# Performance work log

Hardware: AMD Instinct MI355X
Metric: run time of the kernel (lower is better)

## Reference

```python
import jax, jax.numpy as jnp
import numpy as np


def _lstm_cell(x, h, c, Wih, Whh, bih, bhh):
    # PyTorch LSTMCell gate order: i, f, g, o
    g = x @ Wih.T + h @ Whh.T + bih + bhh
    i, f, gg, o = jnp.split(g, 4, axis=-1)
    c = jax.nn.sigmoid(f) * c + jax.nn.sigmoid(i) * jnp.tanh(gg)
    h = jax.nn.sigmoid(o) * jnp.tanh(c)
    return h, c


def setup_inputs() -> dict:
    F, H, B, Te, Td = 64, 128, 1024, 168, 24
    shapes = {
        'input_p_q': (B, Te, F), 'label_p': (B, Td),
        'Wi_w': (H, F), 'Wi_b': (H,), 'We_w': (H, 2 * H),
        'Vd_w': (F, H), 'Vd_b': (F,),
        'enc_Wih': (4 * H, F), 'enc_Whh': (4 * H, H), 'enc_bih': (4 * H,), 'enc_bhh': (4 * H,),
        'mid_Wih': (4 * H, H), 'mid_Whh': (4 * H, H), 'mid_bih': (4 * H,), 'mid_bhh': (4 * H,),
        'Wx_w': (H, H), 'Wx_b': (H,), 'Wh_w': (H, 2 * H),
        'V_w': (1, H), 'V_b': (1,),
        'dec_Wih': (4 * H, H), 'dec_Whh': (4 * H, H), 'dec_bih': (4 * H,), 'dec_bhh': (4 * H,),
        'reg_w': (1, H), 'reg_b': (1,),
    }
    key = jax.random.key(0)
    ks = jax.random.split(key, len(shapes))
    out = {}
    for k, (name, shp) in zip(ks, shapes.items()):
        scale = 1.0 if name in ('input_p_q', 'label_p') else 0.05
        out[name] = jax.random.normal(k, shp, jnp.float32) * scale
    return out


def reference(input_p_q, label_p, Wi_w, Wi_b, We_w, Vd_w, Vd_b,
              enc_Wih, enc_Whh, enc_bih, enc_bhh,
              mid_Wih, mid_Whh, mid_bih, mid_bhh,
              Wx_w, Wx_b, Wh_w, V_w, V_b,
              dec_Wih, dec_Whh, dec_bih, dec_bhh, reg_w, reg_b):
    B, Te, F = input_p_q.shape
    H = Wi_w.shape[0]
    Td = label_p.shape[1]
    h0 = jnp.zeros((B, H), input_p_q.dtype)

    # ---- spatial-attention LSTMCell encoder ----
    xs = jnp.transpose(input_p_q, (1, 0, 2))  # [Te, B, F]

    def enc_step(carry, x_t):
        h, c = carry
        s = jnp.tanh(jnp.concatenate([h, c], axis=1) @ We_w.T
                     + x_t @ Wi_w.T + Wi_b) @ Vd_w.T + Vd_b  # [B, F]
        x_in = x_t * jax.nn.softmax(s, axis=1)
        h, c = _lstm_cell(x_in, h, c, enc_Wih, enc_Whh, enc_bih, enc_bhh)
        return (h, c), h

    _, mid = jax.lax.scan(enc_step, (h0, h0), xs)  # [Te, B, H]

    # ---- single-layer nn.LSTM (LSTM_mid), zero init state ----
    def mid_step(carry, x_t):
        h, c = carry
        h, c = _lstm_cell(x_t, h, c, mid_Wih, mid_Whh, mid_bih, mid_bhh)
        return (h, c), h

    (hi, ci), mid_out = jax.lax.scan(mid_step, (h0, h0), mid)
    mid_out = jnp.transpose(mid_out, (1, 0, 2))  # [B, Te, H]

    # ---- temporal-attention LSTMCell decoder (no softmax on scores, faithful) ----
    wx_mid = mid_out @ Wx_w.T + Wx_b  # [B, Te, H]

    def dec_step(carry, _):
        hi, ci = carry
        q = jnp.concatenate([hi, ci], axis=1) @ Wh_w.T  # [B, H]
        s = jnp.tanh(q[:, None, :] + wx_mid) @ V_w.T + V_b  # [B, Te, 1]
        dec_in = jnp.einsum('bt,bth->bh', s[..., 0], mid_out)
        hi, ci = _lstm_cell(dec_in, hi, ci, dec_Wih, dec_Whh, dec_bih, dec_bhh)
        return (hi, ci), hi

    _, dec = jax.lax.scan(dec_step, (hi, ci), None, length=Td)  # [Td, B, H]
    out = jnp.transpose(dec, (1, 0, 2)) @ reg_w.T + reg_b  # [B, Td, 1]
    return out[..., 0]
```

## Files before the change

kernel.cpp:

```cpp
#include <hip/hip_runtime.h>

#define B_   1024
#define TE   168
#define TD   24
#define F_   64
#define H_   128
#define H2_  256
#define G_   512

#define OFF_WhT    0
#define OFF_dWihT  16384
#define OFF_dWhhT  49152
#define OFF_ENCB   81920
#define OFF_MIDB   82432
#define OFF_DECB   82944
#define OFF_W16    83456
#define W16_We     0
#define W16_Wi     32768
#define W16_Vd     40960
#define W16_eWih   49152
#define W16_eWhh   81920
#define W16_mWih   147456
#define W16_mWhh   212992
#define W16_Wx     278528
#define W16_TOT    294912
#define OFF_MID    230912
#define OFF_WX     (OFF_MID + (B_*TE*H_)/2)
#define OFF_STH    (OFF_WX  + (B_*TE*H_)/2)
#define OFF_STC    (OFF_STH + B_*H_)
#define WS_FLOATS  (OFF_STC + B_*H_)

typedef _Float16 h2 __attribute__((ext_vector_type(2)));
typedef _Float16 h8 __attribute__((ext_vector_type(8)));
typedef _Float16 f16x8 __attribute__((ext_vector_type(8)));
typedef float    f32x4 __attribute__((ext_vector_type(4)));

__device__ __forceinline__ float fexp2(float x) { return __builtin_amdgcn_exp2f(x); }
__device__ __forceinline__ float frcp(float x)  { return __builtin_amdgcn_rcpf(x); }
#define LOG2E 1.4426950408889634f

__device__ __forceinline__ float sigm(float x) {
    return frcp(1.f + fexp2(-LOG2E * x));
}
__device__ __forceinline__ float tanh_fast(float x) {
    float e = fexp2(2.f * LOG2E * x);
    return 1.f - 2.f * frcp(e + 1.f);
}

__device__ __forceinline__ float fdot2(h2 a, h2 b, float c) {
#if __has_builtin(__builtin_amdgcn_fdot2)
    return __builtin_amdgcn_fdot2(a, b, c, false);
#else
    return c + (float)a[0] * (float)b[0] + (float)a[1] * (float)b[1];
#endif
}
__device__ __forceinline__ void fma4(float4& g, const float4 wv, const float s) {
    g.x = __builtin_fmaf(wv.x, s, g.x);
    g.y = __builtin_fmaf(wv.y, s, g.y);
    g.z = __builtin_fmaf(wv.z, s, g.z);
    g.w = __builtin_fmaf(wv.w, s, g.w);
}

#define SH(V,I)  __builtin_shufflevector(V, V, 2*(I), 2*(I)+1)
#define SL(CG)   (4*((CG) + ((CG)>>3)))

#define DPAIR2(LOV, HIV, R0, R1) { \
    h2 c0=SH(LOV,0), c1=SH(LOV,1), c2=SH(LOV,2), c3=SH(LOV,3); \
    h2 c4=SH(HIV,0), c5=SH(HIV,1), c6=SH(HIV,2), c7=SH(HIV,3); \
    a00.x=fdot2(R0,c0,a00.x); a00.y=fdot2(R0,c1,a00.y); a00.z=fdot2(R0,c2,a00.z); a00.w=fdot2(R0,c3,a00.w); \
    a01.x=fdot2(R0,c4,a01.x); a01.y=fdot2(R0,c5,a01.y); a01.z=fdot2(R0,c6,a01.z); a01.w=fdot2(R0,c7,a01.w); \
    a10.x=fdot2(R1,c0,a10.x); a10.y=fdot2(R1,c1,a10.y); a10.z=fdot2(R1,c2,a10.z); a10.w=fdot2(R1,c3,a10.w); \
    a11.x=fdot2(R1,c4,a11.x); a11.y=fdot2(R1,c5,a11.y); a11.z=fdot2(R1,c6,a11.z); a11.w=fdot2(R1,c7,a11.w); \
}

__device__ __forceinline__ f32x4 mfma16(f16x8 a, f16x8 b, f32x4 c) {
    return __builtin_amdgcn_mfma_f32_16x16x32_f16(a, b, c, 0, 0, 0);
}

struct PrepArgs {
    const float *We, *Wi, *Vd, *eWih, *eWhh, *eBih, *eBhh,
                *mWih, *mWhh, *mBih, *mBhh, *Wx, *Wh, *dWih, *dWhh, *dBih, *dBhh;
};

__global__ void prep_kernel(PrepArgs a, float* __restrict__ ws) {
    int sec  = blockIdx.x >> 2;
    int base = (blockIdx.x & 3) * blockDim.x + threadIdx.x;
    const int stride = blockDim.x * 4;
    _Float16* w16 = (_Float16*)(ws + OFF_W16);

    if (sec <= 2) {
        const float* src = (sec == 0) ? a.Wh : (sec == 1) ? a.dWih : a.dWhh;
        int R = (sec == 0) ? 128 : 512;
        int C = (sec == 0) ? 256 : 128;
        int off = (sec == 0) ? OFF_WhT : (sec == 1) ? OFF_dWihT : OFF_dWhhT;
        int n = R * C;
        _Float16* hd = (_Float16*)(ws + off);
        for (int o = base; o < n; o += stride) {
            int r = o % R, c = o / R;
            hd[(c >> 1) * 2 * R + 2 * r + (c & 1)] = (_Float16)src[r * C + c];
        }
    } else if (sec == 3) {
        for (int i = base; i < 512; i += stride) ws[OFF_ENCB + i] = a.eBih[i] + a.eBhh[i];
    } else if (sec == 4) {
        for (int i = base; i < 512; i += stride) ws[OFF_MIDB + i] = a.mBih[i] + a.mBhh[i];
    } else if (sec == 5) {
        for (int i = base; i < 512; i += stride) ws[OFF_DECB + i] = a.dBih[i] + a.dBhh[i];
    } else if (sec <= 13) {
        const int dsto[8] = {W16_We, W16_Wi, W16_Vd, W16_eWih, W16_eWhh, W16_mWih, W16_mWhh, W16_Wx};
        const int cnt[8]  = {32768, 8192, 8192, 32768, 65536, 65536, 65536, 16384};
        const float* srcs[8] = {a.We, a.Wi, a.Vd, a.eWih, a.eWhh, a.mWih, a.mWhh, a.Wx};
        int k = sec - 6;
        const float* s = srcs[k];
        _Float16* d = w16 + dsto[k];
        int n = cnt[k];
        for (int i = base; i < n; i += stride) d[i] = (_Float16)s[i];
    }
}

__global__ __launch_bounds__(512, 1) void enc_kernel(
    const float* __restrict__ x_all,
    const float* __restrict__ Wi_b,
    const float* __restrict__ Vd_b,
    float* __restrict__ ws)
{
    __shared__ __align__(16) _Float16 m1In[16][328];
    __shared__ __align__(16) _Float16 encIn[16][200];
    __shared__ __align__(16) _Float16 avT[16][136];
    __shared__ __align__(16) float sS[16][68];
    __shared__ __align__(16) float xf[16][64];
    __shared__ __align__(16) float cE[16][132];
    __shared__ float bWi[H_], bVd[F_], bE[G_];

    const int tid  = threadIdx.x;
    const int wave = tid >> 6;
    const int lane = tid & 63;
    const int g    = lane >> 4;
    const int cc   = lane & 15;
    const int b0   = blockIdx.x * 16;
    const int col  = wave * 16 + cc;

    for (int i = tid; i < 16 * 328; i += 512) ((_Float16*)m1In)[i]  = (_Float16)0.f;
    for (int i = tid; i < 16 * 200; i += 512) ((_Float16*)encIn)[i] = (_Float16)0.f;
    for (int i = tid; i < 16 * 132; i += 512) ((float*)cE)[i] = 0.f;
    if (tid < H_) bWi[tid] = Wi_b[tid];
    if (tid < F_) bVd[tid] = Vd_b[tid];
    bE[tid] = ws[OFF_ENCB + tid];
    if (tid < 256) {
        int m = tid >> 4, c4 = (tid & 15) * 4;
        float4 v = *(const float4*)&x_all[((size_t)(b0 + m) * TE + 0) * F_ + c4];
        *(float4*)&xf[m][c4] = v;
        m1In[m][256 + c4]     = (_Float16)v.x;
        m1In[m][256 + c4 + 1] = (_Float16)v.y;
        m1In[m][256 + c4 + 2] = (_Float16)v.z;
        m1In[m][256 + c4 + 3] = (_Float16)v.w;
    }

    const _Float16* w16 = (const _Float16*)(ws + OFF_W16);
    f16x8 wWe[8], wWi[2], wVd[4], wIh[4][2], wHh[4][4];
    {
        const _Float16* p = w16 + W16_We + (size_t)col * 256 + 8 * g;
        #pragma unroll
        for (int ks = 0; ks < 8; ++ks) wWe[ks] = *(const f16x8*)(p + ks * 32);
        const _Float16* p2 = w16 + W16_Wi + (size_t)col * 64 + 8 * g;
        wWi[0] = *(const f16x8*)(p2);
        wWi[1] = *(const f16x8*)(p2 + 32);
        if (wave < 4) {
            const _Float16* p3 = w16 + W16_Vd + (size_t)col * 128 + 8 * g;
            #pragma unroll
            for (int ks = 0; ks < 4; ++ks) wVd[ks] = *(const f16x8*)(p3 + ks * 32);
        } else {
            #pragma unroll
            for (int ks = 0; ks < 4; ++ks) wVd[ks] = f16x8{};
        }
        #pragma unroll
        for (int q = 0; q < 4; ++q) {
            const _Float16* pi = w16 + W16_eWih + (size_t)(q * 128 + col) * 64 + 8 * g;
            wIh[q][0] = *(const f16x8*)(pi);
            wIh[q][1] = *(const f16x8*)(pi + 32);
            const _Float16* ph = w16 + W16_eWhh + (size_t)(q * 128 + col) * 128 + 8 * g;
            #pragma unroll
            for (int ks = 0; ks < 4; ++ks) wHh[q][ks] = *(const f16x8*)(ph + ks * 32);
        }
    }
    _Float16* hencG = (_Float16*)(ws + OFF_MID);
    __syncthreads();

    float4 xr = make_float4(0.f, 0.f, 0.f, 0.f);

    for (int t = 0; t < TE; ++t) {
        {
            f16x8 aF[10];
            #pragma unroll
            for (int ks = 0; ks < 10; ++ks)
                aF[ks] = *(const f16x8*)&m1In[cc][ks * 32 + 8 * g];
            f32x4 acc = {0.f, 0.f, 0.f, 0.f};
            #pragma unroll
            for (int ks = 0; ks < 8; ++ks)
                acc = mfma16(aF[ks], wWe[ks], acc);
            acc = mfma16(aF[8], wWi[0], acc);
            acc = mfma16(aF[9], wWi[1], acc);
            float bw = bWi[col];
            #pragma unroll
            for (int r = 0; r < 4; ++r)
                avT[4 * g + r][col] = (_Float16)tanh_fast(acc[r] + bw);
        }
        __syncthreads();

        if (wave < 4) {
            f16x8 aF[4];
            #pragma unroll
            for (int ks = 0; ks < 4; ++ks)
                aF[ks] = *(const f16x8*)&avT[cc][ks * 32 + 8 * g];
            f32x4 acc = {0.f, 0.f, 0.f, 0.f};
            #pragma unroll
            for (int ks = 0; ks < 4; ++ks)
                acc = mfma16(aF[ks], wVd[ks], acc);
            float bv = bVd[col];
            #pragma unroll
            for (int r = 0; r < 4; ++r)
                sS[4 * g + r][col] = acc[r] + bv;
        } else if (t + 1 < TE) {
            int q = tid - 256, m = q >> 4, c4 = (q & 15) * 4;
            xr = *(const float4*)&x_all[((size_t)(b0 + m) * TE + (t + 1)) * F_ + c4];
        }
        __syncthreads();

        {
            int m = tid >> 5, c = tid & 31;
            float v0 = sS[m][c], v1 = sS[m][c + 32];
            float mx = fmaxf(v0, v1);
            #pragma unroll
            for (int off = 16; off > 0; off >>= 1) mx = fmaxf(mx, __shfl_xor(mx, off, 64));
            float e0 = fexp2((v0 - mx) * LOG2E);
            float e1 = fexp2((v1 - mx) * LOG2E);
            float sm = e0 + e1;
            #pragma unroll
            for (int off = 16; off > 0; off >>= 1) sm += __shfl_xor(sm, off, 64);
            float rs = frcp(sm);
            encIn[m][c]      = (_Float16)(xf[m][c]      * e0 * rs);
            encIn[m][c + 32] = (_Float16)(xf[m][c + 32] * e1 * rs);
        }
        __syncthreads();

        f32x4 ge[4];
        {
            f16x8 aF[6];
            #pragma unroll
            for (int ks = 0; ks < 6; ++ks)
                aF[ks] = *(const f16x8*)&encIn[cc][ks * 32 + 8 * g];
            #pragma unroll
            for (int q = 0; q < 4; ++q) {
                f32x4 acc = {0.f, 0.f, 0.f, 0.f};
                acc = mfma16(aF[0], wIh[q][0], acc);
                acc = mfma16(aF[1], wIh[q][1], acc);
                #pragma unroll
                for (int ks = 0; ks < 4; ++ks)
                    acc = mfma16(aF[2 + ks], wHh[q][ks], acc);
                ge[q] = acc;
            }
        }
        __syncthreads();
        {
            float bi = bE[col], bf = bE[col + 128], bg = bE[col + 256], bo = bE[col + 384];
            #pragma unroll
            for (int r = 0; r < 4; ++r) {
                int m = 4 * g + r;
                float gi = ge[0][r] + bi, gf = ge[1][r] + bf,
                      gg = ge[2][r] + bg, go = ge[3][r] + bo;
                float cn = sigm(gf) * cE[m][col] + sigm(gi) * tanh_fast(gg);
                float h  = sigm(go) * tanh_fast(cn);
                cE[m][col] = cn;
                _Float16 hh = (_Float16)h;
                encIn[m][64 + col] = hh;
                m1In[m][col]       = hh;
                m1In[m][128 + col] = (_Float16)cn;
                hencG[((size_t)(b0 + m) * TE + t) * H_ + col] = hh;
            }
            if (tid >= 256 && t + 1 < TE) {
                int q = tid - 256, m = q >> 4, c4 = (q & 15) * 4;
                *(float4*)&xf[m][c4] = xr;
                m1In[m][256 + c4]     = (_Float16)xr.x;
                m1In[m][256 + c4 + 1] = (_Float16)xr.y;
                m1In[m][256 + c4 + 2] = (_Float16)xr.z;
                m1In[m][256 + c4 + 3] = (_Float16)xr.w;
            }
        }
        __syncthreads();
    }
}

__global__ __launch_bounds__(512, 1) void mid_kernel(
    const float* __restrict__ Wx_b,
    float* __restrict__ ws)
{
    __shared__ __align__(16) _Float16 midIn[16][264];
    __shared__ __align__(16) float cM[16][132];
    __shared__ float bM[G_], bWx[H_];

    const int tid  = threadIdx.x;
    const int wave = tid >> 6;
    const int lane = tid & 63;
    const int g    = lane >> 4;
    const int cc   = lane & 15;
    const int b0   = blockIdx.x * 16;
    const int col  = wave * 16 + cc;

    for (int i = tid; i < 16 * 264; i += 512) ((_Float16*)midIn)[i] = (_Float16)0.f;
    for (int i = tid; i < 16 * 132; i += 512) ((float*)cM)[i] = 0.f;
    if (tid < H_) bWx[tid] = Wx_b[tid];
    bM[tid] = ws[OFF_MIDB + tid];

    const _Float16* w16 = (const _Float16*)(ws + OFF_W16);
    f16x8 wIhB[4][4], wHhB[4][4], wWx[4];
    {
        #pragma unroll
        for (int q = 0; q < 4; ++q) {
            const _Float16* pi = w16 + W16_mWih + (size_t)(q * 128 + col) * 128 + 8 * g;
            const _Float16* ph = w16 + W16_mWhh + (size_t)(q * 128 + col) * 128 + 8 * g;
            #pragma unroll
            for (int ks = 0; ks < 4; ++ks) {
                wIhB[q][ks] = *(const f16x8*)(pi + ks * 32);
                wHhB[q][ks] = *(const f16x8*)(ph + ks * 32);
            }
        }
        const _Float16* px = w16 + W16_Wx + (size_t)col * 128 + 8 * g;
        #pragma unroll
        for (int ks = 0; ks < 4; ++ks) wWx[ks] = *(const f16x8*)(px + ks * 32);
    }

    _Float16* hencG = (_Float16*)(ws + OFF_MID);
    _Float16* wxH   = (_Float16*)(ws + OFF_WX);
    __syncthreads();

    if (tid < 256) {
        int m = tid >> 4, s8 = (tid & 15) * 8;
        *(f16x8*)&midIn[m][s8] = *(const f16x8*)&hencG[((size_t)(b0 + m) * TE + 0) * H_ + s8];
    }
    __syncthreads();

    f16x8 hpre = {};
    f32x4 accx = {0.f, 0.f, 0.f, 0.f};

    for (int t = 0; t < TE; ++t) {
        f32x4 gm[4];
        {
            f16x8 aF[8];
            #pragma unroll
            for (int ks = 0; ks < 8; ++ks)
                aF[ks] = *(const f16x8*)&midIn[cc][ks * 32 + 8 * g];
            #pragma unroll
            for (int q = 0; q < 4; ++q) {
                f32x4 acc = {0.f, 0.f, 0.f, 0.f};
                #pragma unroll
                for (int ks = 0; ks < 4; ++ks)
                    acc = mfma16(aF[ks], wIhB[q][ks], acc);
                #pragma unroll
                for (int ks = 0; ks < 4; ++ks)
                    acc = mfma16(aF[4 + ks], wHhB[q][ks], acc);
                gm[q] = acc;
            }
            if (t > 0) {
                f32x4 acc = {0.f, 0.f, 0.f, 0.f};
                #pragma unroll
                for (int ks = 0; ks < 4; ++ks)
                    acc = mfma16(aF[4 + ks], wWx[ks], acc);
                accx = acc;
            }
        }
        if (tid < 256 && t + 1 < TE) {
            int m = tid >> 4, s8 = (tid & 15) * 8;
            hpre = *(const f16x8*)&hencG[((size_t)(b0 + m) * TE + (t + 1)) * H_ + s8];
        }
        __syncthreads();

        {
            float bi = bM[col], bf = bM[col + 128], bg = bM[col + 256], bo = bM[col + 384];
            float bw = bWx[col];
            #pragma unroll
            for (int r = 0; r < 4; ++r) {
                int m = 4 * g + r;
                float gi = gm[0][r] + bi, gf = gm[1][r] + bf,
                      gg = gm[2][r] + bg, go = gm[3][r] + bo;
                float cn = sigm(gf) * cM[m][col] + sigm(gi) * tanh_fast(gg);
                float h  = sigm(go) * tanh_fast(cn);
                cM[m][col] = cn;
                _Float16 hh = (_Float16)h;
                midIn[m][128 + col] = hh;
                hencG[((size_t)(b0 + m) * TE + t) * H_ + col] = hh;
                if (t > 0)
                    wxH[((size_t)(b0 + m) * TE + (t - 1)) * H_ + col] = (_Float16)(accx[r] + bw);
            }
            if (tid < 256 && t + 1 < TE) {
                int m = tid >> 4, s8 = (tid & 15) * 8;
                *(f16x8*)&midIn[m][s8] = hpre;
            }
        }
        __syncthreads();
    }

    {
        f16x8 ax[4];
        #pragma unroll
        for (int ks = 0; ks < 4; ++ks)
            ax[ks] = *(const f16x8*)&midIn[cc][128 + ks * 32 + 8 * g];
        f32x4 acc = {0.f, 0.f, 0.f, 0.f};
        #pragma unroll
        for (int ks = 0; ks < 4; ++ks)
            acc = mfma16(ax[ks], wWx[ks], acc);
        float bw = bWx[col];
        #pragma unroll
        for (int r = 0; r < 4; ++r) {
            int m = 4 * g + r;
            wxH[((size_t)(b0 + m) * TE + (TE - 1)) * H_ + col] = (_Float16)(acc[r] + bw);
        }
    }
    for (int idx = tid; idx < 2048; idx += 512) {
        int m = idx >> 7, j = idx & 127;
        ws[OFF_STH + (b0 + m) * H_ + j] = (float)midIn[m][128 + j];
        ws[OFF_STC + (b0 + m) * H_ + j] = cM[m][j];
    }
}

#define QP_ 132

__global__ __launch_bounds__(512, 2) void dec_kernel(
    const float* __restrict__ Vw_in,
    const float* __restrict__ Vb_in,
    const float* __restrict__ rw_in,
    const float* __restrict__ rb_in,
    const float* __restrict__ ws,
    float* __restrict__ out)
{
    __shared__ __align__(16) float scr[9216];
    __shared__ __align__(16) float hc2[2][H2_];
    __shared__ __align__(16) float qv[2][QP_];
    __shared__ __align__(16) float sb[2][TE];
    __shared__ __align__(16) float dinp[8][2][H_];
    __shared__ float bD[G_], Vw[H_], rw[H_];

    const int tid = threadIdx.x;
    const int b0  = blockIdx.x * 2;
    const float Vb = Vb_in[0], rb = rb_in[0];

    {
        int r = tid >> 8, c = tid & 255;
        hc2[r][c] = (c < H_) ? ws[OFF_STH + (b0 + r) * H_ + c]
                             : ws[OFF_STC + (b0 + r) * H_ + (c - H_)];
    }
    if (tid < H_) { Vw[tid] = Vw_in[tid]; rw[tid] = rw_in[tid]; }
    bD[tid] = ws[OFF_DECB + tid];
    __syncthreads();

    const h8* WhH2  = (const h8*)(ws + OFF_WhT);
    const h8* dWih2 = (const h8*)(ws + OFF_dWihT);
    const h8* dWhh2 = (const h8*)(ws + OFF_dWhhT);
    const h8* wx8   = (const h8*)(ws + OFF_WX);
    typedef _Float16 h4 __attribute__((ext_vector_type(4)));
    const h4* mid4 = (const h4*)(ws + OFF_MID);

    for (int td = 0; td < TD; ++td) {
        {
            int cg = tid & 15, ks = tid >> 4;
            int p0 = ks * 4;
            float4 a00 = make_float4(0.f,0.f,0.f,0.f), a01 = a00, a10 = a00, a11 = a00;
            #pragma unroll
            for (int i = 0; i < 4; ++i) {
                int p = p0 + i;
                h8 lo = WhH2[p * 32 + cg * 2];
                h8 hi = WhH2[p * 32 + cg * 2 + 1];
                h2 r0; r0[0] = (_Float16)hc2[0][2*p]; r0[1] = (_Float16)hc2[0][2*p+1];
                h2 r1; r1[0] = (_Float16)hc2[1][2*p]; r1[1] = (_Float16)hc2[1][2*p+1];
                DPAIR2(lo, hi, r0, r1);
            }
            int sl = SL(cg);
            float* sp = scr + ks * 288;
            *(float4*)(sp +       sl) = a00; *(float4*)(sp +  72 + sl) = a01;
            *(float4*)(sp + 144 + sl) = a10; *(float4*)(sp + 216 + sl) = a11;
        }
        __syncthreads();
        if (tid < 256) {
            int j = tid & 127, r = tid >> 7;
            int e = j & 7, cgj = j >> 3;
            int idx = r * 144 + ((e < 4) ? SL(cgj) + e : 72 + SL(cgj) + (e - 4));
            float v = 0.f;
            #pragma unroll
            for (int ks = 0; ks < 32; ++ks) v += scr[ks * 288 + idx];
            qv[r][j] = v;
        }
        __syncthreads();

        for (int task = tid; task < 2 * TE; task += 512) {
            int r = (task >= TE) ? 1 : 0;
            int tp = task - r * TE;
            const h8* wxr = wx8 + ((size_t)(b0 + r) * TE + tp) * 16;
            float acc = Vb;
            #pragma unroll 4
            for (int kk = 0; kk < 16; ++kk) {
                h8 hv = wxr[kk];
                int j = kk * 8;
                float4 q0 = *(const float4*)&qv[r][j], q1 = *(const float4*)&qv[r][j + 4];
                float4 v0 = *(const float4*)&Vw[j],    v1 = *(const float4*)&Vw[j + 4];
                acc += tanh_fast(q0.x + (float)hv[0]) * v0.x + tanh_fast(q0.y + (float)hv[1]) * v0.y
                     + tanh_fast(q0.z + (float)hv[2]) * v0.z + tanh_fast(q0.w + (float)hv[3]) * v0.w;
                acc += tanh_fast(q1.x + (float)hv[4]) * v1.x + tanh_fast(q1.y + (float)hv[5]) * v1.y
                     + tanh_fast(q1.z + (float)hv[6]) * v1.z + tanh_fast(q1.w + (float)hv[7]) * v1.w;
            }
            sb[r][tp] = acc;
        }
        __syncthreads();

        {
            int ts = tid >> 6, r = (tid >> 5) & 1, cg = tid & 31;
            int t0 = ts * 21;
            float4 a = make_float4(0.f, 0.f, 0.f, 0.f);
            #pragma unroll 3
            for (int tp = t0; tp < t0 + 21; ++tp) {
                float s = sb[r][tp];
                h4 m = mid4[((size_t)(b0 + r) * TE + tp) * 32 + cg];
                float4 mf;
                mf.x = (float)m[0]; mf.y = (float)m[1]; mf.z = (float)m[2]; mf.w = (float)m[3];
                fma4(a, mf, s);
            }
            *(float4*)&dinp[ts][r][cg * 4] = a;
        }
        __syncthreads();
        if (tid < 256) {
            int j = tid & 127, r = tid >> 7;
            qv[r][j] = ((dinp[0][r][j] + dinp[1][r][j]) + (dinp[2][r][j] + dinp[3][r][j]))
                     + ((dinp[4][r][j] + dinp[5][r][j]) + (dinp[6][r][j] + dinp[7][r][j]));
        }
        __syncthreads();

        {
            int cg = tid & 63, ks = tid >> 6;
            int p0 = ks * 8;
            float4 a00 = make_float4(0.f,0.f,0.f,0.f), a01 = a00, a10 = a00, a11 = a00;
            #pragma unroll 4
            for (int i = 0; i < 8; ++i) {
                int p = p0 + i;
                h8 lo = dWih2[p * 128 + cg * 2];
                h8 hi = dWih2[p * 128 + cg * 2 + 1];
                h2 r0; r0[0] = (_Float16)qv[0][2*p]; r0[1] = (_Float16)qv[0][2*p+1];
                h2 r1; r1[0] = (_Float16)qv[1][2*p]; r1[1] = (_Float16)qv[1][2*p+1];
                DPAIR2(lo, hi, r0, r1);
            }
            #pragma unroll 4
            for (int i = 0; i < 8; ++i) {
                int p = p0 + i;
                h8 lo = dWhh2[p * 128 + cg * 2];
                h8 hi = dWhh2[p * 128 + cg * 2 + 1];
                h2 r0; r0[0] = (_Float16)hc2[0][2*p]; r0[1] = (_Float16)hc2[0][2*p+1];
                h2 r1; r1[0] = (_Float16)hc2[1][2*p]; r1[1] = (_Float16)hc2[1][2*p+1];
                DPAIR2(lo, hi, r0, r1);
            }
            int sl = SL(cg);
            float* sp = scr + ks * 1152;
            *(float4*)(sp +       sl) = a00; *(float4*)(sp + 288 + sl) = a01;
            *(float4*)(sp + 576 + sl) = a10; *(float4*)(sp + 864 + sl) = a11;
        }
        __syncthreads();

        if (tid < 256) {
            int j = tid & 127, r = tid >> 7;
            int e = j & 7, cgj = j >> 3;
            int i0, i1, i2, i3;
            {
                int c0 = cgj, c1 = 16 + cgj, c2 = 32 + cgj, c3 = 48 + cgj;
                i0 = (e < 4) ? SL(c0) + e : 288 + SL(c0) + (e - 4);
                i1 = (e < 4) ? SL(c1) + e : 288 + SL(c1) + (e - 4);
                i2 = (e < 4) ? SL(c2) + e : 288 + SL(c2) + (e - 4);
                i3 = (e < 4) ? SL(c3) + e : 288 + SL(c3) + (e - 4);
            }
            const float* sp = scr + r * 576;
            float gi = bD[j], gf = bD[j + 128], gg = bD[j + 256], go = bD[j + 384];
            #pragma unroll
            for (int ks = 0; ks < 8; ++ks) {
                const float* p = sp + ks * 1152;
                gi += p[i0]; gf += p[i1]; gg += p[i2]; go += p[i3];
            }
            float c = sigm(gf) * hc2[r][H_ + j] + sigm(gi) * tanh_fast(gg);
            float h = sigm(go) * tanh_fast(c);
            hc2[r][H_ + j] = c; hc2[r][j] = h;
        }
        __syncthreads();

        if (tid < 128) {
            int r = tid >> 6, lane = tid & 63;
            float v = hc2[r][lane] * rw[lane] + hc2[r][lane + 64] * rw[lane + 64];
            for (int off = 32; off > 0; off >>= 1) v += __shfl_xor(v, off, 64);
            if (lane == 0) out[(b0 + r) * TD + td] = v + rb;
        }
    }
}

extern "C" void kernel_launch(void* const* d_in, const int* in_sizes, int n_in,
                              void* d_out, int out_size, void* d_ws, size_t ws_size,
                              hipStream_t stream)
{
    (void)in_sizes; (void)n_in; (void)out_size;
    if (ws_size < (size_t)WS_FLOATS * sizeof(float)) return;

    const float* x_all = (const float*)d_in[0];
    const float* Wi_b  = (const float*)d_in[3];
    const float* Vd_b  = (const float*)d_in[6];
    const float* Wx_b  = (const float*)d_in[16];
    const float* V_w   = (const float*)d_in[18];
    const float* V_b   = (const float*)d_in[19];
    const float* reg_w = (const float*)d_in[24];
    const float* reg_b = (const float*)d_in[25];
    float* ws  = (float*)d_ws;
    float* out = (float*)d_out;

    PrepArgs pa{
        (const float*)d_in[4],
        (const float*)d_in[2],
        (const float*)d_in[5],
        (const float*)d_in[7],
        (const float*)d_in[8],
        (const float*)d_in[9],
        (const float*)d_in[10],
        (const float*)d_in[11],
        (const float*)d_in[12],
        (const float*)d_in[13],
        (const float*)d_in[14],
        (const float*)d_in[15],
        (const float*)d_in[17],
        (const float*)d_in[20],
        (const float*)d_in[21],
        (const float*)d_in[22],
        (const float*)d_in[23]
    };

    prep_kernel<<<56, 256, 0, stream>>>(pa, ws);
    enc_kernel<<<64, 512, 0, stream>>>(x_all, Wi_b, Vd_b, ws);
    mid_kernel<<<64, 512, 0, stream>>>(Wx_b, ws);
    dec_kernel<<<512, 512, 0, stream>>>(V_w, V_b, reg_w, reg_b, ws, out);
}
```

Baseline: 1.288 ms.

## Fuse encoder and mid LSTM into one producer-consumer kernel with flag sync

New measurement: 1.079 ms. 16.3% less time.

```diff
diff --git a/kernel.cpp b/kernel.cpp
--- a/kernel.cpp
+++ b/kernel.cpp
@@ -82,7 +82,7 @@
                 *mWih, *mWhh, *mBih, *mBhh, *Wx, *Wh, *dWih, *dWhh, *dBih, *dBhh;
 };
 
-__global__ void prep_kernel(PrepArgs a, float* __restrict__ ws) {
+__global__ void prep_kernel(PrepArgs a, float* __restrict__ ws, int* __restrict__ flags) {
     int sec  = blockIdx.x >> 2;
     int base = (blockIdx.x & 3) * blockDim.x + threadIdx.x;
     const int stride = blockDim.x * 4;
@@ -105,6 +105,7 @@
         for (int i = base; i < 512; i += stride) ws[OFF_MIDB + i] = a.mBih[i] + a.mBhh[i];
     } else if (sec == 5) {
         for (int i = base; i < 512; i += stride) ws[OFF_DECB + i] = a.dBih[i] + a.dBhh[i];
+        for (int i = base; i < 64; i += stride) flags[i] = 0;
     } else if (sec <= 13) {
         const int dsto[8] = {W16_We, W16_Wi, W16_Vd, W16_eWih, W16_eWhh, W16_mWih, W16_mWhh, W16_Wx};
         const int cnt[8]  = {32768, 8192, 8192, 32768, 65536, 65536, 65536, 16384};
@@ -117,307 +118,318 @@
     }
 }
 
-__global__ __launch_bounds__(512, 1) void enc_kernel(
+__global__ __launch_bounds__(512, 1) void enc_mid_kernel(
     const float* __restrict__ x_all,
     const float* __restrict__ Wi_b,
     const float* __restrict__ Vd_b,
-    float* __restrict__ ws)
+    const float* __restrict__ Wx_b,
+    float* __restrict__ ws,
+    int* __restrict__ flags)
 {
-    __shared__ __align__(16) _Float16 m1In[16][328];
-    __shared__ __align__(16) _Float16 encIn[16][200];
-    __shared__ __align__(16) _Float16 avT[16][136];
-    __shared__ __align__(16) float sS[16][68];
-    __shared__ __align__(16) float xf[16][64];
-    __shared__ __align__(16) float cE[16][132];
-    __shared__ float bWi[H_], bVd[F_], bE[G_];
-
     const int tid  = threadIdx.x;
     const int wave = tid >> 6;
     const int lane = tid & 63;
     const int g    = lane >> 4;
     const int cc   = lane & 15;
-    const int b0   = blockIdx.x * 16;
+    const int role = blockIdx.x >> 6;
+    const int grp  = blockIdx.x & 63;
+    const int b0   = grp * 16;
     const int col  = wave * 16 + cc;
-
-    for (int i = tid; i < 16 * 328; i += 512) ((_Float16*)m1In)[i]  = (_Float16)0.f;
-    for (int i = tid; i < 16 * 200; i += 512) ((_Float16*)encIn)[i] = (_Float16)0.f;
-    for (int i = tid; i < 16 * 132; i += 512) ((float*)cE)[i] = 0.f;
-    if (tid < H_) bWi[tid] = Wi_b[tid];
-    if (tid < F_) bVd[tid] = Vd_b[tid];
-    bE[tid] = ws[OFF_ENCB + tid];
-    if (tid < 256) {
-        int m = tid >> 4, c4 = (tid & 15) * 4;
-        float4 v = *(const float4*)&x_all[((size_t)(b0 + m) * TE + 0) * F_ + c4];
-        *(float4*)&xf[m][c4] = v;
-        m1In[m][256 + c4]     = (_Float16)v.x;
-        m1In[m][256 + c4 + 1] = (_Float16)v.y;
-        m1In[m][256 + c4 + 2] = (_Float16)v.z;
-        m1In[m][256 + c4 + 3] = (_Float16)v.w;
-    }
-
     const _Float16* w16 = (const _Float16*)(ws + OFF_W16);
-    f16x8 wWe[8], wWi[2], wVd[4], wIh[4][2], wHh[4][4];
-    {
-        const _Float16* p = w16 + W16_We + (size_t)col * 256 + 8 * g;
-        #pragma unroll
-        for (int ks = 0; ks < 8; ++ks) wWe[ks] = *(const f16x8*)(p + ks * 32);
-        const _Float16* p2 = w16 + W16_Wi + (size_t)col * 64 + 8 * g;
-        wWi[0] = *(const f16x8*)(p2);
-        wWi[1] = *(const f16x8*)(p2 + 32);
-        if (wave < 4) {
-            const _Float16* p3 = w16 + W16_Vd + (size_t)col * 128 + 8 * g;
-            #pragma unroll
-            for (int ks = 0; ks < 4; ++ks) wVd[ks] = *(const f16x8*)(p3 + ks * 32);
-        } else {
-            #pragma unroll
-            for (int ks = 0; ks < 4; ++ks) wVd[ks] = f16x8{};
-        }
-        #pragma unroll
-        for (int q = 0; q < 4; ++q) {
-            const _Float16* pi = w16 + W16_eWih + (size_t)(q * 128 + col) * 64 + 8 * g;
-            wIh[q][0] = *(const f16x8*)(pi);
-            wIh[q][1] = *(const f16x8*)(pi + 32);
-            const _Float16* ph = w16 + W16_eWhh + (size_t)(q * 128 + col) * 128 + 8 * g;
-            #pragma unroll
-            for (int ks = 0; ks < 4; ++ks) wHh[q][ks] = *(const f16x8*)(ph + ks * 32);
-        }
-    }
     _Float16* hencG = (_Float16*)(ws + OFF_MID);
-    __syncthreads();
-
-    float4 xr = make_float4(0.f, 0.f, 0.f, 0.f);
-
-    for (int t = 0; t < TE; ++t) {
+
+    if (role == 0) {
+        __shared__ __align__(16) _Float16 m1In[16][328];
+        __shared__ __align__(16) _Float16 encIn[16][200];
+        __shared__ __align__(16) _Float16 avT[16][136];
+        __shared__ __align__(16) float sS[16][68];
+        __shared__ __align__(16) float xf[16][64];
+        __shared__ __align__(16) float cE[16][132];
+        __shared__ float bWi[H_], bVd[F_], bE[G_];
+
+        for (int i = tid; i < 16 * 328; i += 512) ((_Float16*)m1In)[i]  = (_Float16)0.f;
+        for (int i = tid; i < 16 * 200; i += 512) ((_Float16*)encIn)[i] = (_Float16)0.f;
+        for (int i = tid; i < 16 * 132; i += 512) ((float*)cE)[i] = 0.f;
+        if (tid < H_) bWi[tid] = Wi_b[tid];
+        if (tid < F_) bVd[tid] = Vd_b[tid];
+        bE[tid] = ws[OFF_ENCB + tid];
+        if (tid < 256) {
+            int m = tid >> 4, c4 = (tid & 15) * 4;
+            float4 v = *(const float4*)&x_all[((size_t)(b0 + m) * TE + 0) * F_ + c4];
+            *(float4*)&xf[m][c4] = v;
+            m1In[m][256 + c4]     = (_Float16)v.x;
+            m1In[m][256 + c4 + 1] = (_Float16)v.y;
+            m1In[m][256 + c4 + 2] = (_Float16)v.z;
+            m1In[m][256 + c4 + 3] = (_Float16)v.w;
+        }
+
+        f16x8 wWe[8], wWi[2], wVd[4], wIh[4][2], wHh[4][4];
         {
-            f16x8 aF[10];
-            #pragma unroll
-            for (int ks = 0; ks < 10; ++ks)
-                aF[ks] = *(const f16x8*)&m1In[cc][ks * 32 + 8 * g];
+            const _Float16* p = w16 + W16_We + (size_t)col * 256 + 8 * g;
+            #pragma unroll
+            for (int ks = 0; ks < 8; ++ks) wWe[ks] = *(const f16x8*)(p + ks * 32);
+            const _Float16* p2 = w16 + W16_Wi + (size_t)col * 64 + 8 * g;
+            wWi[0] = *(const f16x8*)(p2);
+            wWi[1] = *(const f16x8*)(p2 + 32);
+            if (wave < 4) {
+                const _Float16* p3 = w16 + W16_Vd + (size_t)col * 128 + 8 * g;
+                #pragma unroll
+                for (int ks = 0; ks < 4; ++ks) wVd[ks] = *(const f16x8*)(p3 + ks * 32);
+            } else {
+                #pragma unroll
+                for (int ks = 0; ks < 4; ++ks) wVd[ks] = f16x8{};
+            }
+            #pragma unroll
+            for (int q = 0; q < 4; ++q) {
+                const _Float16* pi = w16 + W16_eWih + (size_t)(q * 128 + col) * 64 + 8 * g;
+                wIh[q][0] = *(const f16x8*)(pi);
+                wIh[q][1] = *(const f16x8*)(pi + 32);
+                const _Float16* ph = w16 + W16_eWhh + (size_t)(q * 128 + col) * 128 + 8 * g;
+                #pragma unroll
+                for (int ks = 0; ks < 4; ++ks) wHh[q][ks] = *(const f16x8*)(ph + ks * 32);
+            }
+        }
+        __syncthreads();
+
+        float4 xr = make_float4(0.f, 0.f, 0.f, 0.f);
+
+        for (int t = 0; t < TE; ++t) {
+            {
+                f16x8 aF[10];
+                #pragma unroll
+                for (int ks = 0; ks < 10; ++ks)
+                    aF[ks] = *(const f16x8*)&m1In[cc][ks * 32 + 8 * g];
+                f32x4 acc = {0.f, 0.f, 0.f, 0.f};
+                #pragma unroll
+                for (int ks = 0; ks < 8; ++ks)
+                    acc = mfma16(aF[ks], wWe[ks], acc);
+                acc = mfma16(aF[8], wWi[0], acc);
+                acc = mfma16(aF[9], wWi[1], acc);
+                float bw = bWi[col];
+                #pragma unroll
+                for (int r = 0; r < 4; ++r)
+                    avT[4 * g + r][col] = (_Float16)tanh_fast(acc[r] + bw);
+            }
+            __syncthreads();
+
+            if (wave < 4) {
+                f16x8 aF[4];
+                #pragma unroll
+                for (int ks = 0; ks < 4; ++ks)
+                    aF[ks] = *(const f16x8*)&avT[cc][ks * 32 + 8 * g];
+                f32x4 acc = {0.f, 0.f, 0.f, 0.f};
+                #pragma unroll
+                for (int ks = 0; ks < 4; ++ks)
+                    acc = mfma16(aF[ks], wVd[ks], acc);
+                float bv = bVd[col];
+                #pragma unroll
+                for (int r = 0; r < 4; ++r)
+                    sS[4 * g + r][col] = acc[r] + bv;
+            } else if (t + 1 < TE) {
+                int q = tid - 256, m = q >> 4, c4 = (q & 15) * 4;
+                xr = *(const float4*)&x_all[((size_t)(b0 + m) * TE + (t + 1)) * F_ + c4];
+            }
+            __syncthreads();
+
+            {
+                int m = tid >> 5, c = tid & 31;
+                float v0 = sS[m][c], v1 = sS[m][c + 32];
+                float mx = fmaxf(v0, v1);
+                #pragma unroll
+                for (int off = 16; off > 0; off >>= 1) mx = fmaxf(mx, __shfl_xor(mx, off, 64));
+                float e0 = fexp2((v0 - mx) * LOG2E);
+                float e1 = fexp2((v1 - mx) * LOG2E);
+                float sm = e0 + e1;
+                #pragma unroll
+                for (int off = 16; off > 0; off >>= 1) sm += __shfl_xor(sm, off, 64);
+                float rs = frcp(sm);
+                encIn[m][c]      = (_Float16)(xf[m][c]      * e0 * rs);
+                encIn[m][c + 32] = (_Float16)(xf[m][c + 32] * e1 * rs);
+            }
+            __syncthreads();
+
+            f32x4 ge[4];
+            {
+                f16x8 aF[6];
+                #pragma unroll
+                for (int ks = 0; ks < 6; ++ks)
+                    aF[ks] = *(const f16x8*)&encIn[cc][ks * 32 + 8 * g];
+                #pragma unroll
+                for (int q = 0; q < 4; ++q) {
+                    f32x4 acc = {0.f, 0.f, 0.f, 0.f};
+                    acc = mfma16(aF[0], wIh[q][0], acc);
+                    acc = mfma16(aF[1], wIh[q][1], acc);
+                    #pragma unroll
+                    for (int ks = 0; ks < 4; ++ks)
+                        acc = mfma16(aF[2 + ks], wHh[q][ks], acc);
+                    ge[q] = acc;
+                }
+            }
+            __syncthreads();
+            {
+                float bi = bE[col], bf = bE[col + 128], bg = bE[col + 256], bo = bE[col + 384];
+                #pragma unroll
+                for (int r = 0; r < 4; ++r) {
+                    int m = 4 * g + r;
+                    float gi = ge[0][r] + bi, gf = ge[1][r] + bf,
+                          gg = ge[2][r] + bg, go = ge[3][r] + bo;
+                    float cn = sigm(gf) * cE[m][col] + sigm(gi) * tanh_fast(gg);
+                    float h  = sigm(go) * tanh_fast(cn);
+                    cE[m][col] = cn;
+                    _Float16 hh = (_Float16)h;
+                    encIn[m][64 + col] = hh;
+                    m1In[m][col]       = hh;
+                    m1In[m][128 + col] = (_Float16)cn;
+                    hencG[((size_t)(b0 + m) * TE + t) * H_ + col] = hh;
+                }
+                if (tid >= 256 && t + 1 < TE) {
+                    int q = tid - 256, m = q >> 4, c4 = (q & 15) * 4;
+                    *(float4*)&xf[m][c4] = xr;
+                    m1In[m][256 + c4]     = (_Float16)xr.x;
+                    m1In[m][256 + c4 + 1] = (_Float16)xr.y;
+                    m1In[m][256 + c4 + 2] = (_Float16)xr.z;
+                    m1In[m][256 + c4 + 3] = (_Float16)xr.w;
+                }
+            }
+            __syncthreads();
+            if (((t + 1) & 7) == 0 && tid == 0)
+                __hip_atomic_store(flags + grp, t + 1, __ATOMIC_RELEASE, __HIP_MEMORY_SCOPE_AGENT);
+        }
+    } else {
+        __shared__ __align__(16) _Float16 midIn[16][264];
+        __shared__ __align__(16) float cM[16][132];
+        __shared__ float bM[G_], bWx[H_];
+
+        for (int i = tid; i < 16 * 264; i += 512) ((_Float16*)midIn)[i] = (_Float16)0.f;
+        for (int i = tid; i < 16 * 132; i += 512) ((float*)cM)[i] = 0.f;
+        if (tid < H_) bWx[tid] = Wx_b[tid];
+        bM[tid] = ws[OFF_MIDB + tid];
+
+        f16x8 wIhB[4][4], wHhB[4][4], wWx[4];
+        {
+            #pragma unroll
+            for (int q = 0; q < 4; ++q) {
+                const _Float16* pi = w16 + W16_mWih + (size_t)(q * 128 + col) * 128 + 8 * g;
+                const _Float16* ph = w16 + W16_mWhh + (size_t)(q * 128 + col) * 128 + 8 * g;
+                #pragma unroll
+                for (int ks = 0; ks < 4; ++ks) {
+                    wIhB[q][ks] = *(const f16x8*)(pi + ks * 32);
+                    wHhB[q][ks] = *(const f16x8*)(ph + ks * 32);
+                }
+            }
+            const _Float16* px = w16 + W16_Wx + (size_t)col * 128 + 8 * g;
+            #pragma unroll
+            for (int ks = 0; ks < 4; ++ks) wWx[ks] = *(const f16x8*)(px + ks * 32);
+        }
+        _Float16* wxH = (_Float16*)(ws + OFF_WX);
+        __syncthreads();
+
+        if (tid == 0) {
+            while (__hip_atomic_load(flags + grp, __ATOMIC_ACQUIRE, __HIP_MEMORY_SCOPE_AGENT) < 8)
+                __builtin_amdgcn_s_sleep(4);
+        }
+        __syncthreads();
+        if (tid < 256) {
+            int m = tid >> 4, s8 = (tid & 15) * 8;
+            *(f16x8*)&midIn[m][s8] = *(const f16x8*)&hencG[((size_t)(b0 + m) * TE + 0) * H_ + s8];
+        }
+        __syncthreads();
+
+        f16x8 hpre = {};
+        f32x4 accx = {0.f, 0.f, 0.f, 0.f};
+
+        for (int t = 0; t < TE; ++t) {
+            const bool pre_ok = (t + 1 < TE) && (((t + 1) & 7) != 0);
+            f32x4 gm[4];
+            {
+                f16x8 aF[8];
+                #pragma unroll
+                for (int ks = 0; ks < 8; ++ks)
+                    aF[ks] = *(const f16x8*)&midIn[cc][ks * 32 + 8 * g];
+                #pragma unroll
+                for (int q = 0; q < 4; ++q) {
+                    f32x4 acc = {0.f, 0.f, 0.f, 0.f};
+                    #pragma unroll
+                    for (int ks = 0; ks < 4; ++ks)
+                        acc = mfma16(aF[ks], wIhB[q][ks], acc);
+                    #pragma unroll
+                    for (int ks = 0; ks < 4; ++ks)
+                        acc = mfma16(aF[4 + ks], wHhB[q][ks], acc);
+                    gm[q] = acc;
+                }
+                if (t > 0) {
+                    f32x4 acc = {0.f, 0.f, 0.f, 0.f};
+                    #pragma unroll
+                    for (int ks = 0; ks < 4; ++ks)
+                        acc = mfma16(aF[4 + ks], wWx[ks], acc);
+                    accx = acc;
+                }
+            }
+            if (tid < 256 && pre_ok) {
+                int m = tid >> 4, s8 = (tid & 15) * 8;
+                hpre = *(const f16x8*)&hencG[((size_t)(b0 + m) * TE + (t + 1)) * H_ + s8];
+            }
+            __syncthreads();
+
+            {
+                float bi = bM[col], bf = bM[col + 128], bg = bM[col + 256], bo = bM[col + 384];
+                float bw = bWx[col];
+                #pragma unroll
+                for (int r = 0; r < 4; ++r) {
+                    int m = 4 * g + r;
+                    float gi = gm[0][r] + bi, gf = gm[1][r] + bf,
+                          gg = gm[2][r] + bg, go = gm[3][r] + bo;
+                    float cn = sigm(gf) * cM[m][col] + sigm(gi) * tanh_fast(gg);
+                    float h  = sigm(go) * tanh_fast(cn);
+                    cM[m][col] = cn;
+                    _Float16 hh = (_Float16)h;
+                    midIn[m][128 + col] = hh;
+                    hencG[((size_t)(b0 + m) * TE + t) * H_ + col] = hh;
+                    if (t > 0)
+                        wxH[((size_t)(b0 + m) * TE + (t - 1)) * H_ + col] = (_Float16)(accx[r] + bw);
+                }
+                if (tid < 256 && pre_ok) {
+                    int m = tid >> 4, s8 = (tid & 15) * 8;
+                    *(f16x8*)&midIn[m][s8] = hpre;
+                }
+            }
+            __syncthreads();
+
+            if (t + 1 < TE && ((t + 1) & 7) == 0) {
+                if (tid == 0) {
+                    while (__hip_atomic_load(flags + grp, __ATOMIC_ACQUIRE, __HIP_MEMORY_SCOPE_AGENT) < t + 9)
+                        __builtin_amdgcn_s_sleep(4);
+                }
+                __syncthreads();
+                if (tid < 256) {
+                    int m = tid >> 4, s8 = (tid & 15) * 8;
+                    *(f16x8*)&midIn[m][s8] = *(const f16x8*)&hencG[((size_t)(b0 + m) * TE + (t + 1)) * H_ + s8];
+                }
+                __syncthreads();
+            }
+        }
+
+        {
+            f16x8 ax[4];
+            #pragma unroll
+            for (int ks = 0; ks < 4; ++ks)
+                ax[ks] = *(const f16x8*)&midIn[cc][128 + ks * 32 + 8 * g];
             f32x4 acc = {0.f, 0.f, 0.f, 0.f};
             #pragma unroll
-            for (int ks = 0; ks < 8; ++ks)
-                acc = mfma16(aF[ks], wWe[ks], acc);
-            acc = mfma16(aF[8], wWi[0], acc);
-            acc = mfma16(aF[9], wWi[1], acc);
-            float bw = bWi[col];
-            #pragma unroll
-            for (int r = 0; r < 4; ++r)
-                avT[4 * g + r][col] = (_Float16)tanh_fast(acc[r] + bw);
-        }
-        __syncthreads();
-
-        if (wave < 4) {
-            f16x8 aF[4];
-            #pragma unroll
             for (int ks = 0; ks < 4; ++ks)
-                aF[ks] = *(const f16x8*)&avT[cc][ks * 32 + 8 * g];
-            f32x4 acc = {0.f, 0.f, 0.f, 0.f};
-            #pragma unroll
-            for (int ks = 0; ks < 4; ++ks)
-                acc = mfma16(aF[ks], wVd[ks], acc);
-            float bv = bVd[col];
-            #pragma unroll
-            for (int r = 0; r < 4; ++r)
-                sS[4 * g + r][col] = acc[r] + bv;
-        } else if (t + 1 < TE) {
-            int q = tid - 256, m = q >> 4, c4 = (q & 15) * 4;
-            xr = *(const float4*)&x_all[((size_t)(b0 + m) * TE + (t + 1)) * F_ + c4];
-        }
-        __syncthreads();
-
-        {
-            int m = tid >> 5, c = tid & 31;
-            float v0 = sS[m][c], v1 = sS[m][c + 32];
-            float mx = fmaxf(v0, v1);
-            #pragma unroll
-            for (int off = 16; off > 0; off >>= 1) mx = fmaxf(mx, __shfl_xor(mx, off, 64));
-            float e0 = fexp2((v0 - mx) * LOG2E);
-            float e1 = fexp2((v1 - mx) * LOG2E);
-            float sm = e0 + e1;
-            #pragma unroll
-            for (int off = 16; off > 0; off >>= 1) sm += __shfl_xor(sm, off, 64);
-            float rs = frcp(sm);
-            encIn[m][c]      = (_Float16)(xf[m][c]      * e0 * rs);
-            encIn[m][c + 32] = (_Float16)(xf[m][c + 32] * e1 * rs);
-        }
-        __syncthreads();
-
-        f32x4 ge[4];
-        {
-            f16x8 aF[6];
-            #pragma unroll
-            for (int ks = 0; ks < 6; ++ks)
-                aF[ks] = *(const f16x8*)&encIn[cc][ks * 32 + 8 * g];
-            #pragma unroll
-            for (int q = 0; q < 4; ++q) {
-                f32x4 acc = {0.f, 0.f, 0.f, 0.f};
-                acc = mfma16(aF[0], wIh[q][0], acc);
-                acc = mfma16(aF[1], wIh[q][1], acc);
-                #pragma unroll
-                for (int ks = 0; ks < 4; ++ks)
-                    acc = mfma16(aF[2 + ks], wHh[q][ks], acc);
-                ge[q] = acc;
-            }
-        }
-        __syncthreads();
-        {
-            float bi = bE[col], bf = bE[col + 128], bg = bE[col + 256], bo = bE[col + 384];
+                acc = mfma16(ax[ks], wWx[ks], acc);
+            float bw = bWx[col];
             #pragma unroll
             for (int r = 0; r < 4; ++r) {
                 int m = 4 * g + r;
-                float gi = ge[0][r] + bi, gf = ge[1][r] + bf,
-                      gg = ge[2][r] + bg, go = ge[3][r] + bo;
-                float cn = sigm(gf) * cE[m][col] + sigm(gi) * tanh_fast(gg);
-                float h  = sigm(go) * tanh_fast(cn);
-                cE[m][col] = cn;
-                _Float16 hh = (_Float16)h;
-                encIn[m][64 + col] = hh;
-                m1In[m][col]       = hh;
-                m1In[m][128 + col] = (_Float16)cn;
-                hencG[((size_t)(b0 + m) * TE + t) * H_ + col] = hh;
-            }
-            if (tid >= 256 && t + 1 < TE) {
-                int q = tid - 256, m = q >> 4, c4 = (q & 15) * 4;
-                *(float4*)&xf[m][c4] = xr;
-                m1In[m][256 + c4]     = (_Float16)xr.x;
-                m1In[m][256 + c4 + 1] = (_Float16)xr.y;
-                m1In[m][256 + c4 + 2] = (_Float16)xr.z;
-                m1In[m][256 + c4 + 3] = (_Float16)xr.w;
-            }
-        }
-        __syncthreads();
-    }
-}
-
-__global__ __launch_bounds__(512, 1) void mid_kernel(
-    const float* __restrict__ Wx_b,
-    float* __restrict__ ws)
-{
-    __shared__ __align__(16) _Float16 midIn[16][264];
-    __shared__ __align__(16) float cM[16][132];
-    __shared__ float bM[G_], bWx[H_];
-
-    const int tid  = threadIdx.x;
-    const int wave = tid >> 6;
-    const int lane = tid & 63;
-    const int g    = lane >> 4;
-    const int cc   = lane & 15;
-    const int b0   = blockIdx.x * 16;
-    const int col  = wave * 16 + cc;
-
-    for (int i = tid; i < 16 * 264; i += 512) ((_Float16*)midIn)[i] = (_Float16)0.f;
-    for (int i = tid; i < 16 * 132; i += 512) ((float*)cM)[i] = 0.f;
-    if (tid < H_) bWx[tid] = Wx_b[tid];
-    bM[tid] = ws[OFF_MIDB + tid];
-
-    const _Float16* w16 = (const _Float16*)(ws + OFF_W16);
-    f16x8 wIhB[4][4], wHhB[4][4], wWx[4];
-    {
-        #pragma unroll
-        for (int q = 0; q < 4; ++q) {
-            const _Float16* pi = w16 + W16_mWih + (size_t)(q * 128 + col) * 128 + 8 * g;
-            const _Float16* ph = w16 + W16_mWhh + (size_t)(q * 128 + col) * 128 + 8 * g;
-            #pragma unroll
-            for (int ks = 0; ks < 4; ++ks) {
-                wIhB[q][ks] = *(const f16x8*)(pi + ks * 32);
-                wHhB[q][ks] = *(const f16x8*)(ph + ks * 32);
-            }
-        }
-        const _Float16* px = w16 + W16_Wx + (size_t)col * 128 + 8 * g;
-        #pragma unroll
-        for (int ks = 0; ks < 4; ++ks) wWx[ks] = *(const f16x8*)(px + ks * 32);
-    }
-
-    _Float16* hencG = (_Float16*)(ws + OFF_MID);
-    _Float16* wxH   = (_Float16*)(ws + OFF_WX);
-    __syncthreads();
-
-    if (tid < 256) {
-        int m = tid >> 4, s8 = (tid & 15) * 8;
-        *(f16x8*)&midIn[m][s8] = *(const f16x8*)&hencG[((size_t)(b0 + m) * TE + 0) * H_ + s8];
-    }
-    __syncthreads();
-
-    f16x8 hpre = {};
-    f32x4 accx = {0.f, 0.f, 0.f, 0.f};
-
-    for (int t = 0; t < TE; ++t) {
-        f32x4 gm[4];
-        {
-            f16x8 aF[8];
-            #pragma unroll
-            for (int ks = 0; ks < 8; ++ks)
-                aF[ks] = *(const f16x8*)&midIn[cc][ks * 32 + 8 * g];
-            #pragma unroll
-            for (int q = 0; q < 4; ++q) {
-                f32x4 acc = {0.f, 0.f, 0.f, 0.f};
-                #pragma unroll
-                for (int ks = 0; ks < 4; ++ks)
-                    acc = mfma16(aF[ks], wIhB[q][ks], acc);
-                #pragma unroll
-                for (int ks = 0; ks < 4; ++ks)
-                    acc = mfma16(aF[4 + ks], wHhB[q][ks], acc);
-                gm[q] = acc;
-            }
-            if (t > 0) {
-                f32x4 acc = {0.f, 0.f, 0.f, 0.f};
-                #pragma unroll
-                for (int ks = 0; ks < 4; ++ks)
-                    acc = mfma16(aF[4 + ks], wWx[ks], acc);
-                accx = acc;
-            }
-        }
-        if (tid < 256 && t + 1 < TE) {
-            int m = tid >> 4, s8 = (tid & 15) * 8;
-            hpre = *(const f16x8*)&hencG[((size_t)(b0 + m) * TE + (t + 1)) * H_ + s8];
-        }
-        __syncthreads();
-
-        {
-            float bi = bM[col], bf = bM[col + 128], bg = bM[col + 256], bo = bM[col + 384];
-            float bw = bWx[col];
-            #pragma unroll
-            for (int r = 0; r < 4; ++r) {
-                int m = 4 * g + r;
-                float gi = gm[0][r] + bi, gf = gm[1][r] + bf,
-                      gg = gm[2][r] + bg, go = gm[3][r] + bo;
-                float cn = sigm(gf) * cM[m][col] + sigm(gi) * tanh_fast(gg);
-                float h  = sigm(go) * tanh_fast(cn);
-                cM[m][col] = cn;
-                _Float16 hh = (_Float16)h;
-                midIn[m][128 + col] = hh;
-                hencG[((size_t)(b0 + m) * TE + t) * H_ + col] = hh;
-                if (t > 0)
-                    wxH[((size_t)(b0 + m) * TE + (t - 1)) * H_ + col] = (_Float16)(accx[r] + bw);
-            }
-            if (tid < 256 && t + 1 < TE) {
-                int m = tid >> 4, s8 = (tid & 15) * 8;
-                *(f16x8*)&midIn[m][s8] = hpre;
-            }
-        }
-        __syncthreads();
-    }
-
-    {
-        f16x8 ax[4];
-        #pragma unroll
-        for (int ks = 0; ks < 4; ++ks)
-            ax[ks] = *(const f16x8*)&midIn[cc][128 + ks * 32 + 8 * g];
-        f32x4 acc = {0.f, 0.f, 0.f, 0.f};
-        #pragma unroll
-        for (int ks = 0; ks < 4; ++ks)
-            acc = mfma16(ax[ks], wWx[ks], acc);
-        float bw = bWx[col];
-        #pragma unroll
-        for (int r = 0; r < 4; ++r) {
-            int m = 4 * g + r;
-            wxH[((size_t)(b0 + m) * TE + (TE - 1)) * H_ + col] = (_Float16)(acc[r] + bw);
-        }
-    }
-    for (int idx = tid; idx < 2048; idx += 512) {
-        int m = idx >> 7, j = idx & 127;
-        ws[OFF_STH + (b0 + m) * H_ + j] = (float)midIn[m][128 + j];
-        ws[OFF_STC + (b0 + m) * H_ + j] = cM[m][j];
+                wxH[((size_t)(b0 + m) * TE + (TE - 1)) * H_ + col] = (_Float16)(acc[r] + bw);
+            }
+        }
+        for (int idx = tid; idx < 2048; idx += 512) {
+            int m = idx >> 7, j = idx & 127;
+            ws[OFF_STH + (b0 + m) * H_ + j] = (float)midIn[m][128 + j];
+            ws[OFF_STC + (b0 + m) * H_ + j] = cM[m][j];
+        }
     }
 }
 
@@ -610,6 +622,7 @@
     const float* reg_b = (const float*)d_in[25];
     float* ws  = (float*)d_ws;
     float* out = (float*)d_out;
+    int* flags = (int*)d_out;
 
     PrepArgs pa{
         (const float*)d_in[4],
@@ -631,8 +644,7 @@
         (const float*)d_in[23]
     };
 
-    prep_kernel<<<56, 256, 0, stream>>>(pa, ws);
-    enc_kernel<<<64, 512, 0, stream>>>(x_all, Wi_b, Vd_b, ws);
-    mid_kernel<<<64, 512, 0, stream>>>(Wx_b, ws);
+    prep_kernel<<<56, 256, 0, stream>>>(pa, ws, flags);
+    enc_mid_kernel<<<128, 512, 0, stream>>>(x_all, Wi_b, Vd_b, Wx_b, ws, flags);
     dec_kernel<<<512, 512, 0, stream>>>(V_w, V_b, reg_w, reg_b, ws, out);
 }
```
